# Kernel tuning notes

Measured on AMD Instinct MI355X. Metric: run time of the kernel, lower is better.

## Reference

```python
import jax, jax.numpy as jnp
import numpy as np

N_NODES = 100000
N_EDGES = 6400000


def setup_inputs() -> dict:
    key = jax.random.key(0)
    k1, k2, k3, k4, k5, k6 = jax.random.split(key, 6)
    x = jax.random.normal(k1, (N_NODES, 20), dtype=jnp.float32)
    edge_index = jax.random.randint(k2, (2, N_EDGES), 0, N_NODES, dtype=jnp.int64)
    # Glorot-style init for GCNConv weights, zero bias (PyG default)
    W1 = jax.random.normal(k3, (20, 16), dtype=jnp.float32) * (1.0 / np.sqrt(20))
    b1 = jnp.zeros((16,), dtype=jnp.float32)
    W2 = jax.random.normal(k4, (16, 2), dtype=jnp.float32) * (1.0 / np.sqrt(16))
    b2 = jnp.zeros((2,), dtype=jnp.float32)
    return {"x": x, "edge_index": edge_index, "W1": W1, "b1": b1, "W2": W2, "b2": b2}


def gcn_conv(x, row, col, W, b, num_nodes):
    # x' = D^{-1/2} (A + I) D^{-1/2} X W + b  (PyG GCNConv with self-loops)
    xw = x @ W  # [N, out]
    ones = jnp.ones_like(row, dtype=xw.dtype)
    deg = jax.ops.segment_sum(ones, row, num_segments=num_nodes)  # [N]
    dinv = jnp.where(deg > 0, jax.lax.rsqrt(deg), 0.0)
    norm = dinv[row] * dinv[col]  # [E+N]
    msg = xw[col] * norm[:, None]  # gather + scale
    out = jax.ops.segment_sum(msg, row, num_segments=num_nodes)  # scatter-add
    return out + b


def reference(x, edge_index, W1, b1, W2, b2):
    num_nodes = x.shape[0]
    self_loops = jnp.arange(num_nodes, dtype=edge_index.dtype)
    row = jnp.concatenate([edge_index[0], self_loops])  # target nodes
    col = jnp.concatenate([edge_index[1], self_loops])  # source nodes
    h = gcn_conv(x, row, col, W1, b1, num_nodes)
    h = jax.nn.relu(h)
    # F.dropout(x, training=self.training): identity in eval mode
    h = gcn_conv(h, row, col, W2, b2, num_nodes)
    return jax.nn.log_softmax(h, axis=1)
```

## Files before the change

kernel.cpp:

```cpp
#include <hip/hip_runtime.h>
#include <math.h>


#define XF 20
#define F1 16
#define F2 2
#define RPB 128
#define KMAX 800
#define KP   784
#define TILE 16384
#define EPT 16
#define NJMAX 400
#define CAP 9216

__device__ __forceinline__ unsigned bf16rne(float f) {
    unsigned u = __float_as_uint(f);
    return (u + 0x7FFFu + ((u >> 16) & 1u)) >> 16;
}
__device__ __forceinline__ float bflo(unsigned w) { return __uint_as_float(w << 16); }
__device__ __forceinline__ float bfhi(unsigned w) { return __uint_as_float(w & 0xFFFF0000u); }

__global__ __launch_bounds__(1024, 8) void passA_kernel(const int* __restrict__ rows,
                                                        const int* __restrict__ cols,
                                                        int* __restrict__ lbt,
                                                        unsigned int* __restrict__ csrtmp,
                                                        int E, int K) {
    __shared__ unsigned int stage[TILE];
    __shared__ int hist[KMAX];
    __shared__ int tsum[1024];
    int t = threadIdx.x;
    int bj = blockIdx.x;
    for (int k = t; k < K; k += 1024) hist[k] = 0;
    __syncthreads();
    int e0 = bj * TILE;
    int e1 = min(e0 + TILE, E);
    int n = e1 - e0;
    int rloc[EPT];
    #pragma unroll
    for (int it = 0; it < EPT; it++) {
        int e = e0 + it * 1024 + t;
        if (e < e1) {
            int r = rows[e];
            rloc[it] = r;
            atomicAdd(&hist[r >> 7], 1);
        }
    }
    __syncthreads();
    int v = (t < K) ? hist[t] : 0;
    tsum[t] = v;
    __syncthreads();
    for (int d = 1; d < 1024; d <<= 1) {
        int u = (t >= d) ? tsum[t - d] : 0;
        __syncthreads();
        tsum[t] += u;
        __syncthreads();
    }
    int run = tsum[t] - v;
    long long lrow = (long long)bj * KP;
    if (t < K) { hist[t] = run; lbt[lrow + t] = run; }
    if (t == 0) lbt[lrow + K] = n;
    __syncthreads();
    #pragma unroll
    for (int it = 0; it < EPT; it++) {
        int e = e0 + it * 1024 + t;
        if (e < e1) {
            int r = rloc[it];
            int c = cols[e];
            int pos = atomicAdd(&hist[r >> 7], 1);
            stage[pos] = ((unsigned int)c << 7) | (unsigned int)(r & 127);
        }
    }
    __syncthreads();
    for (int ss = t; ss < n; ss += 1024)
        csrtmp[(size_t)e0 + ss] = stage[ss];
}

__global__ __launch_bounds__(512) void passB_kernel(const int* __restrict__ lbt,
                                                    const unsigned int* __restrict__ csrtmp,
                                                    unsigned int* __restrict__ csr,
                                                    int2* __restrict__ rp2,
                                                    float* __restrict__ dinv,
                                                    int N, int K, int nj) {
    __shared__ unsigned int stage[CAP];
    __shared__ int segoff[NJMAX];
    __shared__ int stagepos[NJMAX + 1];
    __shared__ int dcnt[RPB];
    __shared__ int rp[RPB];
    __shared__ int cur[RPB];
    __shared__ int tsum[512];
    int b = blockIdx.x, t = threadIdx.x;
    int lo = b << 7;
    if (t < RPB) { dcnt[t] = 0; cur[t] = 0; }
    int la = 0;
    if (t < nj) {
        const int* lp = lbt + (long long)t * KP + b;
        int o0 = lp[0], o1 = lp[1];
        segoff[t] = o0; la = o1 - o0;
    }
    tsum[t] = la;
    __syncthreads();
    for (int d = 1; d < 512; d <<= 1) {
        int u = (t >= d) ? tsum[t - d] : 0;
        __syncthreads();
        tsum[t] += u;
        __syncthreads();
    }
    int run = tsum[t] - la;
    if (t < nj) stagepos[t] = run;
    if (t == 511) stagepos[nj] = tsum[511];
    __syncthreads();
    int cnt = min(stagepos[nj], CAP);
    int sw = t >> 3, ln = t & 7;
    for (int seg = sw; seg < nj; seg += 64) {
        int sp = stagepos[seg];
        int len = stagepos[seg + 1] - sp;
        if (sp + len > CAP) len = max(0, CAP - sp);
        size_t src = (size_t)seg * TILE + segoff[seg];
        for (int e2 = ln; e2 < len; e2 += 8) {
            unsigned int p = csrtmp[src + e2];
            stage[sp + e2] = p;
            atomicAdd(&dcnt[p & 127u], 1);
        }
    }
    __syncthreads();
    int gb = b * CAP;
    if (t < 64) {
        int v0 = dcnt[2 * t], v1 = dcnt[2 * t + 1];
        int ss = v0 + v1;
        int sc = ss;
        #pragma unroll
        for (int d = 1; d < 64; d <<= 1) {
            int u = __shfl_up(sc, d);
            if (t >= d) sc += u;
        }
        int excl = gb + sc - ss;
        rp[2 * t] = excl;
        rp[2 * t + 1] = excl + v0;
        int i0 = lo + 2 * t, i1 = i0 + 1;
        if (i1 < N) {
            ((int4*)rp2)[(lo >> 1) + t] =
                make_int4(excl, excl + v0, excl + v0, excl + v0 + v1);
            dinv[i0] = rsqrtf((float)v0 + 1.0f);
            dinv[i1] = rsqrtf((float)v1 + 1.0f);
        } else if (i0 < N) {
            rp2[i0] = make_int2(excl, excl + v0);
            dinv[i0] = rsqrtf((float)v0 + 1.0f);
        }
    }
    __syncthreads();
    for (int ss = t; ss < cnt; ss += 512) {
        unsigned int p = stage[ss];
        int rr = (int)(p & 127u);
        int dst = rp[rr] + atomicAdd(&cur[rr], 1);
        csr[dst] = p >> 7;
    }
}

__global__ void xw1_kernel(const float* __restrict__ x, const float* __restrict__ W1,
                           const float* __restrict__ dinv, unsigned int* __restrict__ y1h,
                           int N) {
    __shared__ float Ws[XF * F1];
    for (int k = threadIdx.x; k < XF * F1; k += blockDim.x) Ws[k] = W1[k];
    __syncthreads();
    int i = blockIdx.x * blockDim.x + threadIdx.x;
    if (i >= N) return;
    const float4* xv = (const float4*)(x + (size_t)i * XF);
    float xr[XF];
    #pragma unroll
    for (int q = 0; q < 5; q++) {
        float4 v = xv[q];
        xr[q*4+0] = v.x; xr[q*4+1] = v.y; xr[q*4+2] = v.z; xr[q*4+3] = v.w;
    }
    float d = dinv[i];
    float out[F1];
    #pragma unroll
    for (int j = 0; j < F1; j++) {
        float a = 0.f;
        #pragma unroll
        for (int k = 0; k < XF; k++) a += xr[k] * Ws[k * F1 + j];
        out[j] = a * d;
    }
    unsigned int w[8];
    #pragma unroll
    for (int q = 0; q < 8; q++)
        w[q] = bf16rne(out[2*q]) | (bf16rne(out[2*q+1]) << 16);
    uint4* o = (uint4*)(y1h + (size_t)i * 8);
    o[0] = make_uint4(w[0], w[1], w[2], w[3]);
    o[1] = make_uint4(w[4], w[5], w[6], w[7]);
}

__global__ __launch_bounds__(256) void gather16_kernel(const int2* __restrict__ rp2,
                                                       const unsigned int* __restrict__ csr,
                                                       const unsigned int* __restrict__ y1h,
                                                       const float* __restrict__ dinv,
                                                       const float* __restrict__ b1,
                                                       const float* __restrict__ W2,
                                                       float* __restrict__ y2, int N) {
    __shared__ float W2s[F1 * F2];
    if (threadIdx.x < F1 * F2) W2s[threadIdx.x] = W2[threadIdx.x];
    __syncthreads();
    int sub = threadIdx.x >> 5;
    int l = threadIdx.x & 31;
    int i = blockIdx.x * 8 + sub;
    if (i >= N) return;
    int half = l & 1, es = l >> 1;
    int2 se = rp2[i];
    int start = se.x, end = se.y;
    const uint4* Y = (const uint4*)y1h;
    float acc[8] = {0.f, 0.f, 0.f, 0.f, 0.f, 0.f, 0.f, 0.f};
    int slot = start + es;
    int c = (slot < end) ? (int)csr[slot] : 0;
    while (slot < end) {
        int ns = slot + 16;
        int cn = (ns < end) ? (int)csr[ns] : 0;
        uint4 w = Y[(size_t)c * 2 + half];
        acc[0] += bflo(w.x); acc[1] += bfhi(w.x);
        acc[2] += bflo(w.y); acc[3] += bfhi(w.y);
        acc[4] += bflo(w.z); acc[5] += bfhi(w.z);
        acc[6] += bflo(w.w); acc[7] += bfhi(w.w);
        c = cn; slot = ns;
    }
    #pragma unroll
    for (int m = 2; m <= 16; m <<= 1) {
        #pragma unroll
        for (int k = 0; k < 8; k++) acc[k] += __shfl_xor(acc[k], m);
    }
    if (l < 2) {
        float d = dinv[i];
        uint4 w = Y[(size_t)i * 2 + l];
        float self[8] = { bflo(w.x), bfhi(w.x), bflo(w.y), bfhi(w.y),
                          bflo(w.z), bfhi(w.z), bflo(w.w), bfhi(w.w) };
        float4 bl = ((const float4*)b1)[l * 2];
        float4 bh = ((const float4*)b1)[l * 2 + 1];
        float bb[8] = { bl.x, bl.y, bl.z, bl.w, bh.x, bh.y, bh.z, bh.w };
        float p0 = 0.f, p1 = 0.f;
        #pragma unroll
        for (int k = 0; k < 8; k++) {
            float hv = fmaxf(d * (acc[k] + self[k]) + bb[k], 0.f);
            p0 += hv * W2s[(l * 8 + k) * 2];
            p1 += hv * W2s[(l * 8 + k) * 2 + 1];
        }
        float q0 = __shfl_xor(p0, 1);
        float q1 = __shfl_xor(p1, 1);
        if (l == 0)
            ((float2*)y2)[i] = make_float2((p0 + q0) * d, (p1 + q1) * d);
    }
}

__global__ __launch_bounds__(256) void gather2_kernel(const int2* __restrict__ rp2,
                                                      const unsigned int* __restrict__ csr,
                                                      const float* __restrict__ y2,
                                                      const float* __restrict__ dinv,
                                                      const float* __restrict__ b2,
                                                      float* __restrict__ out, int N) {
    int sub = threadIdx.x >> 5;
    int l = threadIdx.x & 31;
    int i = blockIdx.x * 8 + sub;
    if (i >= N) return;
    int2 se = rp2[i];
    int start = se.x, end = se.y;
    float a0 = 0.f, a1 = 0.f;
    int slot = start + l;
    int c = (slot < end) ? (int)csr[slot] : 0;
    while (slot < end) {
        int ns = slot + 32;
        int cn = (ns < end) ? (int)csr[ns] : 0;
        float2 v = ((const float2*)y2)[c];
        a0 += v.x;
        a1 += v.y;
        c = cn; slot = ns;
    }
    #pragma unroll
    for (int m = 16; m > 0; m >>= 1) {
        a0 += __shfl_xor(a0, m);
        a1 += __shfl_xor(a1, m);
    }
    if (l == 0) {
        float d = dinv[i];
        float2 yi = ((const float2*)y2)[i];
        float v0 = d * (a0 + yi.x) + b2[0];
        float v1 = d * (a1 + yi.y) + b2[1];
        float mm = fmaxf(v0, v1);
        float lse = mm + logf(expf(v0 - mm) + expf(v1 - mm));
        ((float2*)out)[i] = make_float2(v0 - lse, v1 - lse);
    }
}

static inline size_t align256(size_t x) { return (x + 255) & ~(size_t)255; }

extern "C" void kernel_launch(void* const* d_in, const int* in_sizes, int n_in,
                              void* d_out, int out_size, void* d_ws, size_t ws_size,
                              hipStream_t stream) {
    const float* x  = (const float*)d_in[0];
    const int*   ei = (const int*)d_in[1];
    const float* W1 = (const float*)d_in[2];
    const float* b1 = (const float*)d_in[3];
    const float* W2 = (const float*)d_in[4];
    const float* b2 = (const float*)d_in[5];
    float* out = (float*)d_out;

    const int N = in_sizes[0] / XF;
    const int E = in_sizes[1] / 2;
    const int* rows = ei;
    const int* cols = ei + E;
    const int K = (N + RPB - 1) >> 7;
    const int nj = (E + TILE - 1) / TILE;

    char* ws = (char*)d_ws;
    size_t off = 0;
    int2*  rp2     = (int2*)(ws + off);  off = align256(off + (size_t)N * 8);
    float* dinv    = (float*)(ws + off); off = align256(off + (size_t)N * 4);
    int*   lbt     = (int*)(ws + off);   off = align256(off + (size_t)nj * KP * 4);
    unsigned int* csr = (unsigned int*)(ws + off);
    off = align256(off + (size_t)K * CAP * 4);
    size_t tmp0 = off;
    unsigned int* csrtmp = (unsigned int*)(ws + tmp0);
    unsigned int* y1h = (unsigned int*)(ws + tmp0);
    float* y2 = (float*)(ws + align256(tmp0 + (size_t)N * 8 * 4));

    const int B = 256;
    const int nbN = (N + B - 1) / B;
    const int nbW = (N + 7) / 8;

    passA_kernel<<<nj, 1024, 0, stream>>>(rows, cols, lbt, csrtmp, E, K);
    passB_kernel<<<K, 512, 0, stream>>>(lbt, csrtmp, csr, rp2, dinv, N, K, nj);
    xw1_kernel<<<nbN, B, 0, stream>>>(x, W1, dinv, y1h, N);
    gather16_kernel<<<nbW, B, 0, stream>>>(rp2, csr, y1h, dinv, b1, W2, y2, N);
    gather2_kernel<<<nbW, B, 0, stream>>>(rp2, csr, y2, dinv, b2, out, N);
}
```

Baseline: 240.4 us.

## Use wavefront shuffle scans and balanced per-thread gather in CSR build passes

Replaces the shared-memory Hillis-Steele block scans in passA and passB with two-level wavefront shuffle scans, removing many block-wide barriers. PassB's segment copy now gives each thread an even contiguous slice of the staged edges, finds the starting segment by binary search, and batches four loads before the LDS writes and atomics. This replaces the fixed eight-lanes-per-segment mapping, which was imbalanced across segments. CAP is reduced and launch bounds set to 8 to fit more blocks per CU, at the risk of more edges overflowing the staging capacity.

```diff
diff --git a/kernel.cpp b/kernel.cpp
--- a/kernel.cpp
+++ b/kernel.cpp
@@ -11,7 +11,7 @@
 #define TILE 16384
 #define EPT 16
 #define NJMAX 400
-#define CAP 9216
+#define CAP 8960
 
 __device__ __forceinline__ unsigned bf16rne(float f) {
     unsigned u = __float_as_uint(f);
@@ -27,7 +27,7 @@
                                                         int E, int K) {
     __shared__ unsigned int stage[TILE];
     __shared__ int hist[KMAX];
-    __shared__ int tsum[1024];
+    __shared__ int wsum[16];
     int t = threadIdx.x;
     int bj = blockIdx.x;
     for (int k = t; k < K; k += 1024) hist[k] = 0;
@@ -47,15 +47,27 @@
     }
     __syncthreads();
     int v = (t < K) ? hist[t] : 0;
-    tsum[t] = v;
-    __syncthreads();
-    for (int d = 1; d < 1024; d <<= 1) {
-        int u = (t >= d) ? tsum[t - d] : 0;
-        __syncthreads();
-        tsum[t] += u;
-        __syncthreads();
-    }
-    int run = tsum[t] - v;
+    int w = t >> 6, lane = t & 63;
+    int sc = v;
+    #pragma unroll
+    for (int d = 1; d < 64; d <<= 1) {
+        int u = __shfl_up(sc, d);
+        if (lane >= d) sc += u;
+    }
+    if (lane == 63) wsum[w] = sc;
+    __syncthreads();
+    if (t < 16) {
+        int vv = wsum[t];
+        int s2 = vv;
+        #pragma unroll
+        for (int d = 1; d < 16; d <<= 1) {
+            int u = __shfl_up(s2, d);
+            if (t >= d) s2 += u;
+        }
+        wsum[t] = s2 - vv;
+    }
+    __syncthreads();
+    int run = sc - v + wsum[w];
     long long lrow = (long long)bj * KP;
     if (t < K) { hist[t] = run; lbt[lrow + t] = run; }
     if (t == 0) lbt[lrow + K] = n;
@@ -75,19 +87,19 @@
         csrtmp[(size_t)e0 + ss] = stage[ss];
 }
 
-__global__ __launch_bounds__(512) void passB_kernel(const int* __restrict__ lbt,
-                                                    const unsigned int* __restrict__ csrtmp,
-                                                    unsigned int* __restrict__ csr,
-                                                    int2* __restrict__ rp2,
-                                                    float* __restrict__ dinv,
-                                                    int N, int K, int nj) {
+__global__ __launch_bounds__(512, 8) void passB_kernel(const int* __restrict__ lbt,
+                                                       const unsigned int* __restrict__ csrtmp,
+                                                       unsigned int* __restrict__ csr,
+                                                       int2* __restrict__ rp2,
+                                                       float* __restrict__ dinv,
+                                                       int N, int K, int nj) {
     __shared__ unsigned int stage[CAP];
     __shared__ int segoff[NJMAX];
     __shared__ int stagepos[NJMAX + 1];
     __shared__ int dcnt[RPB];
     __shared__ int rp[RPB];
     __shared__ int cur[RPB];
-    __shared__ int tsum[512];
+    __shared__ int wsum[8];
     int b = blockIdx.x, t = threadIdx.x;
     int lo = b << 7;
     if (t < RPB) { dcnt[t] = 0; cur[t] = 0; }
@@ -97,29 +109,65 @@
         int o0 = lp[0], o1 = lp[1];
         segoff[t] = o0; la = o1 - o0;
     }
-    tsum[t] = la;
-    __syncthreads();
-    for (int d = 1; d < 512; d <<= 1) {
-        int u = (t >= d) ? tsum[t - d] : 0;
-        __syncthreads();
-        tsum[t] += u;
-        __syncthreads();
-    }
-    int run = tsum[t] - la;
+    int w = t >> 6, lane = t & 63;
+    int sc = la;
+    #pragma unroll
+    for (int d = 1; d < 64; d <<= 1) {
+        int u = __shfl_up(sc, d);
+        if (lane >= d) sc += u;
+    }
+    if (lane == 63) wsum[w] = sc;
+    __syncthreads();
+    if (t < 8) {
+        int vv = wsum[t];
+        int s2 = vv;
+        #pragma unroll
+        for (int d = 1; d < 8; d <<= 1) {
+            int u = __shfl_up(s2, d);
+            if (t >= d) s2 += u;
+        }
+        wsum[t] = s2 - vv;
+    }
+    __syncthreads();
+    int run = sc - la + wsum[w];
     if (t < nj) stagepos[t] = run;
-    if (t == 511) stagepos[nj] = tsum[511];
+    if (t == 511) stagepos[nj] = run + la;
     __syncthreads();
     int cnt = min(stagepos[nj], CAP);
-    int sw = t >> 3, ln = t & 7;
-    for (int seg = sw; seg < nj; seg += 64) {
-        int sp = stagepos[seg];
-        int len = stagepos[seg + 1] - sp;
-        if (sp + len > CAP) len = max(0, CAP - sp);
-        size_t src = (size_t)seg * TILE + segoff[seg];
-        for (int e2 = ln; e2 < len; e2 += 8) {
-            unsigned int p = csrtmp[src + e2];
-            stage[sp + e2] = p;
-            atomicAdd(&dcnt[p & 127u], 1);
+    int per = (cnt + 511) >> 9;
+    int lo_i = t * per;
+    int hi_i = min(cnt, lo_i + per);
+    if (lo_i < hi_i) {
+        int sl = 0, sh = nj;
+        while (sh - sl > 1) {
+            int mid = (sl + sh) >> 1;
+            if (stagepos[mid] <= lo_i) sl = mid; else sh = mid;
+        }
+        int seg = sl;
+        int idx = lo_i;
+        while (idx < hi_i) {
+            int addr[4];
+            unsigned int pv[4];
+            int i2 = idx, s2 = seg;
+            int na = 0;
+            #pragma unroll
+            for (int u = 0; u < 4; u++) {
+                if (i2 < hi_i) {
+                    while (i2 >= stagepos[s2 + 1]) s2++;
+                    addr[u] = s2 * TILE + segoff[s2] + (i2 - stagepos[s2]);
+                    i2++; na++;
+                }
+            }
+            #pragma unroll
+            for (int u = 0; u < 4; u++)
+                if (u < na) pv[u] = csrtmp[addr[u]];
+            #pragma unroll
+            for (int u = 0; u < 4; u++)
+                if (u < na) {
+                    stage[idx + u] = pv[u];
+                    atomicAdd(&dcnt[pv[u] & 127u], 1);
+                }
+            idx = i2; seg = s2;
         }
     }
     __syncthreads();
@@ -127,13 +175,13 @@
     if (t < 64) {
         int v0 = dcnt[2 * t], v1 = dcnt[2 * t + 1];
         int ss = v0 + v1;
-        int sc = ss;
+        int sc2 = ss;
         #pragma unroll
         for (int d = 1; d < 64; d <<= 1) {
-            int u = __shfl_up(sc, d);
-            if (t >= d) sc += u;
-        }
-        int excl = gb + sc - ss;
+            int u = __shfl_up(sc2, d);
+            if (t >= d) sc2 += u;
+        }
+        int excl = gb + sc2 - ss;
         rp[2 * t] = excl;
         rp[2 * t + 1] = excl + v0;
         int i0 = lo + 2 * t, i1 = i0 + 1;
```

Result: slower. 248.5 us (+3.4%).
